# Kernel tuning notes

Hardware: AMD Instinct MI355X
Metric: run time of the kernel (lower is better)

## Reference

```python
import jax, jax.numpy as jnp
import numpy as np

NUM_INSTANCES = 8
NUM_HEADS = 4
EPS = 1e-12  # F.normalize eps


def _l2norm(t):
    # F.normalize(t, dim=-1): t / max(||t||_2, eps) along last axis
    n = jnp.sqrt(jnp.sum(t * t, axis=-1, keepdims=True))
    return t / jnp.maximum(n, EPS)


def setup_inputs() -> dict:
    key = jax.random.key(0)
    ks = jax.random.split(key, 10)
    B, C, H, W = 8, 256, 32, 32
    I = NUM_INSTANCES
    s = 0.05
    return {
        "x": jax.random.normal(ks[0], (B, C, H, W), dtype=jnp.float32),
        "w_inst": jax.random.normal(ks[1], (I, C), dtype=jnp.float32) * s,
        "b_inst": jnp.zeros((I,), dtype=jnp.float32),
        "w_q": jax.random.normal(ks[2], (C, C), dtype=jnp.float32) * s,
        "b_q": jnp.zeros((C,), dtype=jnp.float32),
        "w_k": jax.random.normal(ks[3], (C, C), dtype=jnp.float32) * s,
        "b_k": jnp.zeros((C,), dtype=jnp.float32),
        "w_v": jax.random.normal(ks[4], (C, C), dtype=jnp.float32) * s,
        "b_v": jnp.zeros((C,), dtype=jnp.float32),
    }


def reference(x, w_inst, b_inst, w_q, b_q, w_k, b_k, w_v, b_v):
    B, C, H, W = x.shape
    HW = H * W
    hd = C // NUM_HEADS
    scale = 1.0 / jnp.sqrt(jnp.float32(hd))

    # instance_conv (1x1) + softmax over instance axis
    inst = jnp.einsum('ic,bchw->bihw', w_inst, x) + b_inst[None, :, None, None]
    inst = jax.nn.softmax(inst, axis=1)          # [B, I, H, W]
    masks = jnp.transpose(inst, (1, 0, 2, 3))    # [I, B, H, W] for scan

    def step(acc, mask):                          # mask: [B, H, W]
        feat = (x * mask[:, None]).reshape(B, C, HW)  # masked features
        q = (jnp.einsum('oc,bcn->bon', w_q, feat) + b_q[:, None]).reshape(B, NUM_HEADS, hd, HW)
        k = (jnp.einsum('oc,bcn->bon', w_k, feat) + b_k[:, None]).reshape(B, NUM_HEADS, hd, HW)
        v = (jnp.einsum('oc,bcn->bon', w_v, feat) + b_v[:, None]).reshape(B, NUM_HEADS, hd, HW)
        q = _l2norm(q)
        k = _l2norm(k)
        scores = jnp.einsum('bhci,bhcj->bhij', q, k) * scale  # [B,h,HW,HW]
        attn = jax.nn.softmax(scores, axis=-1)
        att = jnp.einsum('bhij,bhcj->bhci', attn, v).reshape(B, C, H, W)
        return acc + att * mask[:, None], None

    out, _ = jax.lax.scan(step, jnp.zeros_like(x), masks)
    return out
```

## Files before the change

kernel.cpp:

```cpp
#include <hip/hip_runtime.h>
#include <hip/hip_fp16.h>

#define NB 8
#define NC 256
#define NHW 1024
#define NI 8
#define NH 4
#define HD 64
#define EPS 1e-12f
#define QSC  64.0f
#define QSCI 0.015625f

typedef _Float16 f16;
typedef __attribute__((ext_vector_type(8))) _Float16 half8;
typedef __attribute__((ext_vector_type(4))) float floatx4;

union H8 { half8 h8; __half2 h2[4]; uint4 u4; f16 e[8]; };
union H4 { uint2 u2; __half2 h2[2]; f16 e[4]; };
union PK { __half2 h2; unsigned u; };

__device__ __forceinline__ void gll16(const void* g, void* l) {
    __builtin_amdgcn_global_load_lds(
        (const __attribute__((address_space(1))) unsigned int*)g,
        (__attribute__((address_space(3))) unsigned int*)l, 16, 0, 0);
}

__global__ __launch_bounds__(256) void k_mask_part(
    const float* __restrict__ x, const float* __restrict__ w_inst,
    float* __restrict__ part_m, f16* __restrict__ xt)
{
    __shared__ __align__(16) f16 xls[32][264];
    int nt = blockIdx.x, b = blockIdx.y, cc = blockIdx.z;
    int tid = threadIdx.x;
    int n = nt*256 + tid;
    const float* xp = x + ((size_t)(b*NC + cc*32))*NHW + n;
    const float* wp = w_inst + cc*32;
    float acc[NI] = {};
#pragma unroll
    for (int c = 0; c < 32; ++c) {
        float xv = xp[(size_t)c*NHW];
        xls[c][tid] = (f16)xv;
#pragma unroll
        for (int i = 0; i < NI; ++i) acc[i] = fmaf(wp[i*NC + c], xv, acc[i]);
    }
#pragma unroll
    for (int i = 0; i < NI; ++i)
        part_m[((size_t)(cc*NI + i)*NB + b)*NHW + n] = acc[i];
    __syncthreads();
#pragma unroll
    for (int it = 0; it < 4; ++it) {
        int r = (tid >> 2) + it*64;
        int c8 = (tid & 3)*8;
        H8 v;
#pragma unroll
        for (int i = 0; i < 8; ++i) v.e[i] = xls[c8 + i][r];
        *(uint4*)(xt + ((size_t)(b*NHW + nt*256 + r))*NC + cc*32 + c8) = v.u4;
    }
}

__global__ __launch_bounds__(256) void k_gemm_mfma(
    const f16* __restrict__ xt,
    const float* __restrict__ wq, const float* __restrict__ wk, const float* __restrict__ wv,
    f16* __restrict__ Gqt, f16* __restrict__ Gkt, f16* __restrict__ Gv)
{
    __shared__ __align__(16) char glds[30720];
    int tid = threadIdx.x;
    int nt = blockIdx.x, ot = blockIdx.y;
    int m = blockIdx.z >> 3, b = blockIdx.z & 7;
    const float* wsel = (m == 0) ? wq : (m == 1) ? wk : wv;
    int o0 = ot*64;
    int w = tid >> 6, lane = tid & 63, quad = lane >> 4, l15 = lane & 15;
    const f16* xb = xt + (size_t)b*NHW*NC + (size_t)nt*128*NC;
    f16* wt0 = (f16*)glds;
    f16* xt0 = (f16*)(glds + 10240);
    int srow = tid >> 2, scol = (tid & 3)*8;

    floatx4 acc[2][4];
#pragma unroll
    for (int nm=0;nm<2;nm++)
#pragma unroll
        for (int om=0;om<4;om++){ acc[nm][om][0]=0.f; acc[nm][om][1]=0.f;
                                  acc[nm][om][2]=0.f; acc[nm][om][3]=0.f; }
    {
        float4 a4 = *(const float4*)(wsel + (size_t)(o0+srow)*NC + scol);
        float4 b4 = *(const float4*)(wsel + (size_t)(o0+srow)*NC + scol + 4);
        H8 hw;
        hw.h2[0] = __floats2half2_rn(a4.x, a4.y); hw.h2[1] = __floats2half2_rn(a4.z, a4.w);
        hw.h2[2] = __floats2half2_rn(b4.x, b4.y); hw.h2[3] = __floats2half2_rn(b4.z, b4.w);
        *(uint4*)&wt0[(0*64 + srow)*40 + scol] = hw.u4;
        *(uint4*)&xt0[(0*128 + srow)*40 + scol]    = *(const uint4*)(xb + (size_t)srow*NC + scol);
        *(uint4*)&xt0[(0*128 + 64+srow)*40 + scol] = *(const uint4*)(xb + (size_t)(64+srow)*NC + scol);
    }
    for (int k = 0; k < 8; ++k) {
        int p = k & 1;
        __syncthreads();
        if (k < 7) {
            int q = 1 - p, kc = (k+1)*32;
            float4 a4 = *(const float4*)(wsel + (size_t)(o0+srow)*NC + kc + scol);
            float4 b4 = *(const float4*)(wsel + (size_t)(o0+srow)*NC + kc + scol + 4);
            H8 hw;
            hw.h2[0] = __floats2half2_rn(a4.x, a4.y); hw.h2[1] = __floats2half2_rn(a4.z, a4.w);
            hw.h2[2] = __floats2half2_rn(b4.x, b4.y); hw.h2[3] = __floats2half2_rn(b4.z, b4.w);
            *(uint4*)&wt0[(q*64 + srow)*40 + scol] = hw.u4;
            *(uint4*)&xt0[(q*128 + srow)*40 + scol]    = *(const uint4*)(xb + (size_t)srow*NC + kc + scol);
            *(uint4*)&xt0[(q*128 + 64+srow)*40 + scol] = *(const uint4*)(xb + (size_t)(64+srow)*NC + kc + scol);
        }
        H8 wa[4], xa[2];
#pragma unroll
        for (int om = 0; om < 4; ++om)
            wa[om].u4 = *(const uint4*)&wt0[(p*64 + om*16 + l15)*40 + quad*8];
#pragma unroll
        for (int nm = 0; nm < 2; ++nm)
            xa[nm].u4 = *(const uint4*)&xt0[(p*128 + w*32 + nm*16 + l15)*40 + quad*8];
#pragma unroll
        for (int nm = 0; nm < 2; ++nm)
#pragma unroll
            for (int om = 0; om < 4; ++om)
                acc[nm][om] = __builtin_amdgcn_mfma_f32_16x16x32_f16(wa[om].h8, xa[nm].h8, acc[nm][om], 0, 0, 0);
    }
    __syncthreads();
    if (m < 2) {
        f16* lt = (f16*)glds;
#pragma unroll
        for (int nm = 0; nm < 2; ++nm)
#pragma unroll
            for (int om = 0; om < 4; ++om) {
                H4 pk;
#pragma unroll
                for (int r = 0; r < 4; ++r) pk.e[r] = (f16)acc[nm][om][r];
                *(uint2*)&lt[(size_t)(w*32 + nm*16 + l15)*72 + om*16 + quad*4] = pk.u2;
            }
        __syncthreads();
        f16* dst = (m == 0) ? Gqt : Gkt;
#pragma unroll
        for (int it = 0; it < 4; ++it) {
            int row = (tid >> 3) + it*32;
            int c8 = (tid & 7)*8;
            uint4 v = *(const uint4*)&lt[(size_t)row*72 + c8];
            *(uint4*)(dst + ((size_t)(b*NHW + nt*128 + row))*NC + o0 + c8) = v;
        }
    } else {
        f16* lv = (f16*)glds;
#pragma unroll
        for (int nm = 0; nm < 2; ++nm)
#pragma unroll
            for (int om = 0; om < 4; ++om)
#pragma unroll
                for (int r = 0; r < 4; ++r)
                    lv[(size_t)(om*16 + quad*4 + r)*136 + w*32 + nm*16 + l15] = (f16)acc[nm][om][r];
        __syncthreads();
#pragma unroll
        for (int it = 0; it < 4; ++it) {
            int row = (tid >> 4) + it*16;
            int n8 = (tid & 15)*8;
            uint4 v = *(const uint4*)&lv[(size_t)row*136 + n8];
            *(uint4*)(Gv + ((size_t)(b*NC + o0 + row))*NHW + nt*128 + n8) = v;
        }
    }
}

__global__ __launch_bounds__(256) void k_norm_mask(
    const float* __restrict__ part_m, const float* __restrict__ b_inst,
    const f16* __restrict__ Gqt, const f16* __restrict__ Gkt,
    const float* __restrict__ bq, const float* __restrict__ bk,
    float* __restrict__ masks, float* __restrict__ part_nq, float* __restrict__ part_nk)
{
    __shared__ float lg[NI][32];
    __shared__ __align__(16) float m_s[NI][32];
    int nc = blockIdx.x, b = blockIdx.y;
    int tid = threadIdx.x;
    int n0 = nc*32;
    {
        int nl = tid & 31, i = tid >> 5;
        float s = b_inst[i];
#pragma unroll
        for (int cc = 0; cc < 8; ++cc)
            s += part_m[((size_t)(cc*NI + i)*NB + b)*NHW + n0 + nl];
        lg[i][nl] = s;
    }
    __syncthreads();
    {
        int nl = tid & 31, i = tid >> 5;
        float mx = lg[0][nl];
#pragma unroll
        for (int k = 1; k < NI; ++k) mx = fmaxf(mx, lg[k][nl]);
        float ssum = 0.f;
#pragma unroll
        for (int k = 0; k < NI; ++k) ssum += __expf(lg[k][nl] - mx);
        float mv = __expf(lg[i][nl] - mx) / ssum;
        m_s[i][nl] = mv;
        masks[((size_t)i*NB + b)*NHW + n0 + nl] = mv;
    }
    __syncthreads();
    int c = tid;
    float bqv = bq[c], bkv = bk[c];
    const f16* gq = Gqt + ((size_t)b*NHW + n0)*NC + c;
    const f16* gk = Gkt + ((size_t)b*NHW + n0)*NC + c;
    float aq[NI] = {}, ak[NI] = {};
#pragma unroll
    for (int t4 = 0; t4 < 32; t4 += 4) {
        float g1[4], g2[4];
#pragma unroll
        for (int r = 0; r < 4; ++r) {
            g1[r] = (float)gq[(size_t)(t4 + r)*NC];
            g2[r] = (float)gk[(size_t)(t4 + r)*NC];
        }
#pragma unroll
        for (int i = 0; i < NI; ++i) {
            float4 mm4 = *(const float4*)&m_s[i][t4];
            float mm[4] = {mm4.x, mm4.y, mm4.z, mm4.w};
#pragma unroll
            for (int r = 0; r < 4; ++r) {
                float e = fmaf(mm[r], g1[r], bqv); aq[i] = fmaf(e, e, aq[i]);
                e = fmaf(mm[r], g2[r], bkv);       ak[i] = fmaf(e, e, ak[i]);
            }
        }
    }
#pragma unroll
    for (int i = 0; i < NI; ++i) {
        part_nq[((size_t)(nc*NI + i)*NB + b)*NC + c] = aq[i];
        part_nk[((size_t)(nc*NI + i)*NB + b)*NC + c] = ak[i];
    }
}

__global__ __launch_bounds__(256) void k_norm_fin(
    const float* __restrict__ part_nq, const float* __restrict__ part_nk,
    float* __restrict__ scale_q, float* __restrict__ scale_k)
{
    int b = blockIdx.x, i = blockIdx.y, c = threadIdx.x;
    float sq = 0.f, sk = 0.f;
#pragma unroll
    for (int nc = 0; nc < 32; ++nc) {
        sq += part_nq[((size_t)(nc*NI + i)*NB + b)*NC + c];
        sk += part_nk[((size_t)(nc*NI + i)*NB + b)*NC + c];
    }
    scale_q[((size_t)i*NB + b)*NC + c] = 0.125f / fmaxf(sqrtf(sq), EPS);
    scale_k[((size_t)i*NB + b)*NC + c] = 1.0f   / fmaxf(sqrtf(sk), EPS);
}

__global__ __launch_bounds__(512,2) void k_attn13(
    const f16* __restrict__ Gqt, const f16* __restrict__ Gkt, const f16* __restrict__ Gv,
    const float* __restrict__ masks,
    const float* __restrict__ bq, const float* __restrict__ bv,
    const float* __restrict__ scale_q, const float* __restrict__ scale_k,
    float* __restrict__ out)
{
    __shared__ __align__(16) char lds[36864];
    f16*   KH = (f16*)lds;
    f16*   VH = (f16*)(lds + 16384);
    float* MI = (float*)(lds + 32768);

    int tid = threadIdx.x, bid = blockIdx.x;
    int b = bid & 7, qt = (bid >> 3) & 31, h = bid >> 8;
    int qt0 = qt*32, c0 = h*HD;
    int w = tid >> 6, lane = tid & 63, quad = lane >> 4, l15 = lane & 15;

    H8 graw[2][2];
    const f16* gqp = Gqt + ((size_t)b*NHW + qt0)*NC + c0;
#pragma unroll
    for (int qi = 0; qi < 2; ++qi)
#pragma unroll
        for (int ks = 0; ks < 2; ++ks)
            graw[qi][ks].u4 = *(const uint4*)(gqp + (size_t)(qi*16 + l15)*NC + ks*32 + quad*8);
    float mqf[2];
#pragma unroll
    for (int qi = 0; qi < 2; ++qi)
        mqf[qi] = masks[((size_t)w*NB + b)*NHW + qt0 + qi*16 + l15];
    H8 qa[2][2];
#pragma unroll
    for (int ks = 0; ks < 2; ++ks) {
        int cb = c0 + ks*32 + quad*8;
        float4 bq0 = *(const float4*)(bq + cb);
        float4 bq1 = *(const float4*)(bq + cb + 4);
        const float* sqg = scale_q + ((size_t)w*NB + b)*NC;
        const float* skg = scale_k + ((size_t)w*NB + b)*NC;
        float4 s0 = *(const float4*)(sqg + cb);
        float4 s1 = *(const float4*)(sqg + cb + 4);
        float4 t0 = *(const float4*)(skg + cb);
        float4 t1 = *(const float4*)(skg + cb + 4);
        float ss[8] = {s0.x*t0.x*QSC, s0.y*t0.y*QSC, s0.z*t0.z*QSC, s0.w*t0.w*QSC,
                       s1.x*t1.x*QSC, s1.y*t1.y*QSC, s1.z*t1.z*QSC, s1.w*t1.w*QSC};
        float bb[8] = {bq0.x*ss[0], bq0.y*ss[1], bq0.z*ss[2], bq0.w*ss[3],
                       bq1.x*ss[4], bq1.y*ss[5], bq1.z*ss[6], bq1.w*ss[7]};
        __half2 sh[4], bh[4];
#pragma unroll
        for (int t = 0; t < 4; ++t) {
            sh[t] = __floats2half2_rn(ss[2*t], ss[2*t+1]);
            bh[t] = __floats2half2_rn(bb[2*t], bb[2*t+1]);
        }
#pragma unroll
        for (int qi = 0; qi < 2; ++qi) {
            __half2 mq2 = __float2half2_rn(mqf[qi]);
#pragma unroll
            for (int t = 0; t < 4; ++t)
                qa[qi][ks].h2[t] = __hfma2(mq2, __hmul2(graw[qi][ks].h2[t], sh[t]), bh[t]);
        }
    }

    int kjr = tid >> 3, kdc = (tid & 7) ^ (kjr & 7);
    const f16* kgb = Gkt + (size_t)b*NHW*NC + c0 + kdc*8;
    int vcr = tid >> 3, vdc = (tid & 7) ^ (vcr & 7);
    const f16* vgb = Gv + ((size_t)(b*NC + c0 + vcr))*NHW + vdc*8;
    const float* mgb = masks + ((size_t)(tid >> 4)*NB + b)*NHW + (tid & 15)*4;

    floatx4 acc[4][2];
#pragma unroll
    for (int cm=0;cm<4;cm++)
#pragma unroll
        for (int qi=0;qi<2;qi++) { acc[cm][qi][0]=0.f; acc[cm][qi][1]=0.f;
                                   acc[cm][qi][2]=0.f; acc[cm][qi][3]=0.f; }
    float l[2] = {};

    gll16(kgb + (size_t)kjr*NC, KH + tid*8);
    gll16(vgb,                  VH + tid*8);
    if (tid < 128) gll16(mgb, MI + tid*4);
    __syncthreads();

    int p = 0;
    for (int j0 = 0; j0 < NHW; j0 += 64) {
        int jn = (j0 + 64) & (NHW - 1);
        gll16(kgb + (size_t)(jn + kjr)*NC, KH + (p^1)*4096 + tid*8);
        gll16(vgb + jn,                    VH + (p^1)*4096 + tid*8);
        if (tid < 128) gll16(mgb + jn, MI + (p^1)*512 + tid*4);

        const f16* kh = KH + p*4096;
        const f16* vh = VH + p*4096;
        const float* mi = MI + p*512;

#pragma unroll
        for (int half = 0; half < 2; ++half) {
            unsigned pw[2][2][2];
#pragma unroll
            for (int jm2 = 0; jm2 < 2; ++jm2) {
                int jm = half*2 + jm2;
                int krow = jm*16 + l15;
                H8 ka0, ka1;
                ka0.u4 = *(const uint4*)&kh[krow*64 + ((quad       ^ (l15 & 7))*8)];
                ka1.u4 = *(const uint4*)&kh[krow*64 + (((4 + quad) ^ (l15 & 7))*8)];
                floatx4 s0 = {0.f,0.f,0.f,0.f}, s1 = {0.f,0.f,0.f,0.f};
                s0 = __builtin_amdgcn_mfma_f32_16x16x32_f16(ka0.h8, qa[0][0].h8, s0, 0, 0, 0);
                s0 = __builtin_amdgcn_mfma_f32_16x16x32_f16(ka1.h8, qa[0][1].h8, s0, 0, 0, 0);
                s1 = __builtin_amdgcn_mfma_f32_16x16x32_f16(ka0.h8, qa[1][0].h8, s1, 0, 0, 0);
                s1 = __builtin_amdgcn_mfma_f32_16x16x32_f16(ka1.h8, qa[1][1].h8, s1, 0, 0, 0);
                float4 mj4 = *(const float4*)&mi[w*64 + jm*16 + quad*4];
                float mj[4] = {mj4.x, mj4.y, mj4.z, mj4.w};
                float p0[4], p1[4];
#pragma unroll
                for (int r = 0; r < 4; ++r) {
                    float mq = mj[r]*QSCI;
                    float e0 = __expf(s0[r]*mq); l[0] += e0; p0[r] = e0*mj[r];
                    float e1 = __expf(s1[r]*mq); l[1] += e1; p1[r] = e1*mj[r];
                }
                PK k0, k1, k2, k3;
                k0.h2 = __floats2half2_rn(p0[0], p0[1]); k1.h2 = __floats2half2_rn(p0[2], p0[3]);
                k2.h2 = __floats2half2_rn(p1[0], p1[1]); k3.h2 = __floats2half2_rn(p1[2], p1[3]);
                pw[0][jm2][0] = k0.u; pw[0][jm2][1] = k1.u;
                pw[1][jm2][0] = k2.u; pw[1][jm2][1] = k3.u;
            }
            H8 pb[2];
#pragma unroll
            for (int qi = 0; qi < 2; ++qi) {
                unsigned a = pw[qi][0][0], bx = pw[qi][0][1];
                unsigned c = pw[qi][1][0], d  = pw[qi][1][1];
                asm("v_permlane32_swap_b32 %0, %1" : "+v"(a),  "+v"(c));
                asm("v_permlane16_swap_b32 %0, %1" : "+v"(a),  "+v"(c));
                asm("v_permlane32_swap_b32 %0, %1" : "+v"(bx), "+v"(d));
                asm("v_permlane16_swap_b32 %0, %1" : "+v"(bx), "+v"(d));
                H8 t; t.u4.x = a; t.u4.y = bx; t.u4.z = c; t.u4.w = d;
                pb[qi] = t;
            }
#pragma unroll
            for (int cm = 0; cm < 4; ++cm) {
                H8 va;
                va.u4 = *(const uint4*)&vh[(cm*16 + l15)*64 + (((half*4 + quad) ^ (l15 & 7))*8)];
                acc[cm][0] = __builtin_amdgcn_mfma_f32_16x16x32_f16(va.h8, pb[0].h8, acc[cm][0], 0, 0, 0);
                acc[cm][1] = __builtin_amdgcn_mfma_f32_16x16x32_f16(va.h8, pb[1].h8, acc[cm][1], 0, 0, 0);
            }
        }
        __syncthreads();
        p ^= 1;
    }

    float f[2];
#pragma unroll
    for (int qi = 0; qi < 2; ++qi) {
        float lv = l[qi];
        lv += __shfl_xor(lv, 16, 64);
        lv += __shfl_xor(lv, 32, 64);
        f[qi] = mqf[qi] / lv;
    }
    float* rb = (float*)lds + (size_t)(w & 3)*2304;
    if (w < 4) {
#pragma unroll
        for (int cm = 0; cm < 4; ++cm)
#pragma unroll
            for (int qi = 0; qi < 2; ++qi)
#pragma unroll
                for (int r = 0; r < 4; ++r)
                    rb[(cm*16 + quad*4 + r)*36 + qi*16 + l15] = f[qi]*acc[cm][qi][r];
    }
    __syncthreads();
    if (w >= 4) {
#pragma unroll
        for (int cm = 0; cm < 4; ++cm)
#pragma unroll
            for (int qi = 0; qi < 2; ++qi)
#pragma unroll
                for (int r = 0; r < 4; ++r)
                    rb[(cm*16 + quad*4 + r)*36 + qi*16 + l15] += f[qi]*acc[cm][qi][r];
    }
    __syncthreads();
    int cc2 = tid >> 3, qg = (tid & 7)*4;
    float bvv = bv[c0 + cc2];
    const float* b0 = (const float*)lds;
    float4 v0 = *(const float4*)&b0[cc2*36 + qg];
    float4 v1 = *(const float4*)&b0[2304 + cc2*36 + qg];
    float4 v2 = *(const float4*)&b0[4608 + cc2*36 + qg];
    float4 v3 = *(const float4*)&b0[6912 + cc2*36 + qg];
    float4 v;
    v.x = v0.x + v1.x + v2.x + v3.x + bvv;
    v.y = v0.y + v1.y + v2.y + v3.y + bvv;
    v.z = v0.z + v1.z + v2.z + v3.z + bvv;
    v.w = v0.w + v1.w + v2.w + v3.w + bvv;
    *(float4*)(out + ((size_t)(b*NC + c0 + cc2))*NHW + qt0 + qg) = v;
}

extern "C" void kernel_launch(void* const* d_in, const int* in_sizes, int n_in,
                              void* d_out, int out_size, void* d_ws, size_t ws_size,
                              hipStream_t stream)
{
    const float* x      = (const float*)d_in[0];
    const float* w_inst = (const float*)d_in[1];
    const float* b_inst = (const float*)d_in[2];
    const float* wq = (const float*)d_in[3];
    const float* bq = (const float*)d_in[4];
    const float* wk = (const float*)d_in[5];
    const float* bk = (const float*)d_in[6];
    const float* wv = (const float*)d_in[7];
    const float* bv = (const float*)d_in[8];
    float* out = (float*)d_out;

    float* masks   = (float*)d_ws;
    float* scale_q = masks + (size_t)NI*NB*NHW;
    float* scale_k = scale_q + (size_t)NI*NB*NC;
    f16*   Gqt     = (f16*)(scale_k + (size_t)NI*NB*NC);
    f16*   Gkt     = Gqt + (size_t)NB*NHW*NC;
    f16*   Gv      = Gkt + (size_t)NB*NHW*NC;
    f16*   xt      = Gv + (size_t)NB*NC*NHW;
    float* part_m  = (float*)(xt + (size_t)NB*NHW*NC);
    float* part_nq = part_m + (size_t)8*NI*NB*NHW;
    float* part_nk = part_nq + (size_t)32*NI*NB*NC;

    k_mask_part<<<dim3(4, NB, 8), 256, 0, stream>>>(x, w_inst, part_m, xt);
    k_gemm_mfma<<<dim3(8, 4, 24), 256, 0, stream>>>(xt, wq, wk, wv, Gqt, Gkt, Gv);
    k_norm_mask<<<dim3(32, NB), 256, 0, stream>>>(part_m, b_inst, Gqt, Gkt, bq, bk,
                                                  masks, part_nq, part_nk);
    k_norm_fin<<<dim3(NB, NI), 256, 0, stream>>>(part_nq, part_nk, scale_q, scale_k);
    k_attn13<<<dim3(1024), 512, 0, stream>>>(Gqt, Gkt, Gv, masks, bq, bv,
                                             scale_q, scale_k, out);
}
```

Measured before the change: 203.0 us.

## Fuse mask softmax into x transpose kernel and collapse norm reduction passes

```diff
diff --git a/kernel.cpp b/kernel.cpp
--- a/kernel.cpp
+++ b/kernel.cpp
@@ -25,37 +25,51 @@
         (__attribute__((address_space(3))) unsigned int*)l, 16, 0, 0);
 }
 
-__global__ __launch_bounds__(256) void k_mask_part(
+__global__ __launch_bounds__(256) void k_mask_xt(
     const float* __restrict__ x, const float* __restrict__ w_inst,
-    float* __restrict__ part_m, f16* __restrict__ xt)
+    const float* __restrict__ b_inst,
+    float* __restrict__ masks, f16* __restrict__ xt)
 {
     __shared__ __align__(16) f16 xls[32][264];
-    int nt = blockIdx.x, b = blockIdx.y, cc = blockIdx.z;
+    int nt = blockIdx.x, b = blockIdx.y;
     int tid = threadIdx.x;
     int n = nt*256 + tid;
-    const float* xp = x + ((size_t)(b*NC + cc*32))*NHW + n;
-    const float* wp = w_inst + cc*32;
+    const float* xp = x + ((size_t)b*NC)*NHW + n;
     float acc[NI] = {};
-#pragma unroll
-    for (int c = 0; c < 32; ++c) {
-        float xv = xp[(size_t)c*NHW];
-        xls[c][tid] = (f16)xv;
-#pragma unroll
-        for (int i = 0; i < NI; ++i) acc[i] = fmaf(wp[i*NC + c], xv, acc[i]);
-    }
+    for (int cc = 0; cc < 8; ++cc) {
+#pragma unroll
+        for (int c = 0; c < 32; ++c) {
+            float xv = xp[(size_t)(cc*32 + c)*NHW];
+            xls[c][tid] = (f16)xv;
+#pragma unroll
+            for (int i = 0; i < NI; ++i)
+                acc[i] = fmaf(w_inst[i*NC + cc*32 + c], xv, acc[i]);
+        }
+        __syncthreads();
+#pragma unroll
+        for (int it = 0; it < 4; ++it) {
+            int r = (tid >> 2) + it*64;
+            int c8 = (tid & 3)*8;
+            H8 v;
+#pragma unroll
+            for (int i = 0; i < 8; ++i) v.e[i] = xls[c8 + i][r];
+            *(uint4*)(xt + ((size_t)(b*NHW + nt*256 + r))*NC + cc*32 + c8) = v.u4;
+        }
+        __syncthreads();
+    }
+    float s[NI];
+#pragma unroll
+    for (int i = 0; i < NI; ++i) s[i] = acc[i] + b_inst[i];
+    float mx = s[0];
+#pragma unroll
+    for (int i = 1; i < NI; ++i) mx = fmaxf(mx, s[i]);
+    float ssum = 0.f;
+#pragma unroll
+    for (int i = 0; i < NI; ++i) { s[i] = __expf(s[i] - mx); ssum += s[i]; }
+    float inv = 1.0f / ssum;
 #pragma unroll
     for (int i = 0; i < NI; ++i)
-        part_m[((size_t)(cc*NI + i)*NB + b)*NHW + n] = acc[i];
-    __syncthreads();
-#pragma unroll
-    for (int it = 0; it < 4; ++it) {
-        int r = (tid >> 2) + it*64;
-        int c8 = (tid & 3)*8;
-        H8 v;
-#pragma unroll
-        for (int i = 0; i < 8; ++i) v.e[i] = xls[c8 + i][r];
-        *(uint4*)(xt + ((size_t)(b*NHW + nt*256 + r))*NC + cc*32 + c8) = v.u4;
-    }
+        masks[((size_t)i*NB + b)*NHW + n] = s[i]*inv;
 }
 
 __global__ __launch_bounds__(256) void k_gemm_mfma(
@@ -159,46 +173,23 @@
     }
 }
 
-__global__ __launch_bounds__(256) void k_norm_mask(
-    const float* __restrict__ part_m, const float* __restrict__ b_inst,
+__global__ __launch_bounds__(256) void k_scale(
+    const float* __restrict__ masks,
     const f16* __restrict__ Gqt, const f16* __restrict__ Gkt,
     const float* __restrict__ bq, const float* __restrict__ bk,
-    float* __restrict__ masks, float* __restrict__ part_nq, float* __restrict__ part_nk)
+    float* __restrict__ scale_q, float* __restrict__ scale_k)
 {
-    __shared__ float lg[NI][32];
-    __shared__ __align__(16) float m_s[NI][32];
-    int nc = blockIdx.x, b = blockIdx.y;
-    int tid = threadIdx.x;
-    int n0 = nc*32;
-    {
-        int nl = tid & 31, i = tid >> 5;
-        float s = b_inst[i];
-#pragma unroll
-        for (int cc = 0; cc < 8; ++cc)
-            s += part_m[((size_t)(cc*NI + i)*NB + b)*NHW + n0 + nl];
-        lg[i][nl] = s;
-    }
-    __syncthreads();
-    {
-        int nl = tid & 31, i = tid >> 5;
-        float mx = lg[0][nl];
-#pragma unroll
-        for (int k = 1; k < NI; ++k) mx = fmaxf(mx, lg[k][nl]);
-        float ssum = 0.f;
-#pragma unroll
-        for (int k = 0; k < NI; ++k) ssum += __expf(lg[k][nl] - mx);
-        float mv = __expf(lg[i][nl] - mx) / ssum;
-        m_s[i][nl] = mv;
-        masks[((size_t)i*NB + b)*NHW + n0 + nl] = mv;
-    }
-    __syncthreads();
-    int c = tid;
+    int b = blockIdx.x, i = blockIdx.y;
+    int c = threadIdx.x;
     float bqv = bq[c], bkv = bk[c];
-    const f16* gq = Gqt + ((size_t)b*NHW + n0)*NC + c;
-    const f16* gk = Gkt + ((size_t)b*NHW + n0)*NC + c;
-    float aq[NI] = {}, ak[NI] = {};
-#pragma unroll
-    for (int t4 = 0; t4 < 32; t4 += 4) {
+    const f16* gq = Gqt + (size_t)b*NHW*NC + c;
+    const f16* gk = Gkt + (size_t)b*NHW*NC + c;
+    const float* mp = masks + ((size_t)i*NB + b)*NHW;
+    float aq = 0.f, ak = 0.f;
+#pragma unroll 8
+    for (int t4 = 0; t4 < NHW; t4 += 4) {
+        float4 mm4 = *(const float4*)(mp + t4);
+        float mm[4] = {mm4.x, mm4.y, mm4.z, mm4.w};
         float g1[4], g2[4];
 #pragma unroll
         for (int r = 0; r < 4; ++r) {
@@ -206,36 +197,13 @@
             g2[r] = (float)gk[(size_t)(t4 + r)*NC];
         }
 #pragma unroll
-        for (int i = 0; i < NI; ++i) {
-            float4 mm4 = *(const float4*)&m_s[i][t4];
-            float mm[4] = {mm4.x, mm4.y, mm4.z, mm4.w};
-#pragma unroll
-            for (int r = 0; r < 4; ++r) {
-                float e = fmaf(mm[r], g1[r], bqv); aq[i] = fmaf(e, e, aq[i]);
-                e = fmaf(mm[r], g2[r], bkv);       ak[i] = fmaf(e, e, ak[i]);
-            }
-        }
-    }
-#pragma unroll
-    for (int i = 0; i < NI; ++i) {
-        part_nq[((size_t)(nc*NI + i)*NB + b)*NC + c] = aq[i];
-        part_nk[((size_t)(nc*NI + i)*NB + b)*NC + c] = ak[i];
-    }
-}
-
-__global__ __launch_bounds__(256) void k_norm_fin(
-    const float* __restrict__ part_nq, const float* __restrict__ part_nk,
-    float* __restrict__ scale_q, float* __restrict__ scale_k)
-{
-    int b = blockIdx.x, i = blockIdx.y, c = threadIdx.x;
-    float sq = 0.f, sk = 0.f;
-#pragma unroll
-    for (int nc = 0; nc < 32; ++nc) {
-        sq += part_nq[((size_t)(nc*NI + i)*NB + b)*NC + c];
-        sk += part_nk[((size_t)(nc*NI + i)*NB + b)*NC + c];
-    }
-    scale_q[((size_t)i*NB + b)*NC + c] = 0.125f / fmaxf(sqrtf(sq), EPS);
-    scale_k[((size_t)i*NB + b)*NC + c] = 1.0f   / fmaxf(sqrtf(sk), EPS);
+        for (int r = 0; r < 4; ++r) {
+            float e = fmaf(mm[r], g1[r], bqv); aq = fmaf(e, e, aq);
+            e = fmaf(mm[r], g2[r], bkv);       ak = fmaf(e, e, ak);
+        }
+    }
+    scale_q[((size_t)i*NB + b)*NC + c] = 0.125f / fmaxf(sqrtf(aq), EPS);
+    scale_k[((size_t)i*NB + b)*NC + c] = 1.0f   / fmaxf(sqrtf(ak), EPS);
 }
 
 __global__ __launch_bounds__(512,2) void k_attn13(
@@ -447,15 +415,10 @@
     f16*   Gkt     = Gqt + (size_t)NB*NHW*NC;
     f16*   Gv      = Gkt + (size_t)NB*NHW*NC;
     f16*   xt      = Gv + (size_t)NB*NC*NHW;
-    float* part_m  = (float*)(xt + (size_t)NB*NHW*NC);
-    float* part_nq = part_m + (size_t)8*NI*NB*NHW;
-    float* part_nk = part_nq + (size_t)32*NI*NB*NC;
-
-    k_mask_part<<<dim3(4, NB, 8), 256, 0, stream>>>(x, w_inst, part_m, xt);
+
+    k_mask_xt<<<dim3(4, NB), 256, 0, stream>>>(x, w_inst, b_inst, masks, xt);
     k_gemm_mfma<<<dim3(8, 4, 24), 256, 0, stream>>>(xt, wq, wk, wv, Gqt, Gkt, Gv);
-    k_norm_mask<<<dim3(32, NB), 256, 0, stream>>>(part_m, b_inst, Gqt, Gkt, bq, bk,
-                                                  masks, part_nq, part_nk);
-    k_norm_fin<<<dim3(NB, NI), 256, 0, stream>>>(part_nq, part_nk, scale_q, scale_k);
+    k_scale<<<dim3(NB, NI), 256, 0, stream>>>(masks, Gqt, Gkt, bq, bk, scale_q, scale_k);
     k_attn13<<<dim3(1024), 512, 0, stream>>>(Gqt, Gkt, Gv, masks, bq, bv,
                                              scale_q, scale_k, out);
 }
```

New measurement: 280.3 us. 38.1% more time.
